# Kernel optimization log

Hardware: AMD Instinct MI355X
Metric: run time of the kernel (lower is better)

Reference implementation:

```python
import jax, jax.numpy as jnp
import numpy as np

INF = 10000000000000.0
HEADS = 12
HEAD_SIZE = 64

def _rope_tables(seqlen, dim):
    inv_freq = 1.0 / (10000.0 ** (jnp.arange(0, dim, 2, dtype=jnp.float32) / dim))
    t = jnp.arange(seqlen, dtype=jnp.float32)
    freqs = t[:, None] * inv_freq[None, :]            # [S, d/2]
    # unsqueeze_dim=-2 -> [S, 1, d/2] to broadcast over heads
    return jnp.sin(freqs)[:, None, :], jnp.cos(freqs)[:, None, :]

def _apply_rope(t, sin, cos):
    # t: [B, S, H, D]; sin/cos: [S, 1, D/2]
    t1, t2 = t[..., 0::2], t[..., 1::2]
    out = jnp.stack([t1 * cos - t2 * sin, t1 * sin + t2 * cos], axis=-1)
    return out.reshape(t.shape)

def setup_inputs() -> dict:
    key = jax.random.key(0)
    k1, k2 = jax.random.split(key)
    B, S, Hd = 32, 512, 1024
    x = jax.random.normal(k1, (B, S, Hd), dtype=jnp.float32)
    W = jax.random.normal(k2, (Hd, HEADS * 2 * HEAD_SIZE), dtype=jnp.float32) * (1.0 / np.sqrt(Hd))
    b = jnp.zeros((HEADS * 2 * HEAD_SIZE,), dtype=jnp.float32)
    attention_mask = jnp.ones((B, S), dtype=jnp.int32)
    return {"x": x, "W": W, "b": b, "attention_mask": attention_mask}

def reference(x, W, b, attention_mask):
    B, S, _ = x.shape
    proj = x @ W + b                                   # [B, S, H*2*D]
    proj = proj.reshape(B, S, HEADS, 2, HEAD_SIZE)
    qw, kw = proj[..., 0, :], proj[..., 1, :]          # [B, S, H, D]
    sin, cos = _rope_tables(S, HEAD_SIZE)
    qw = _apply_rope(qw, sin, cos)
    kw = _apply_rope(kw, sin, cos)
    logits = jnp.einsum('bmhd,bnhd->bhmn', qw, kw)     # [B, H, S, S]
    am = attention_mask.astype(logits.dtype)
    pad_mask = 1.0 - am[:, None, None, :] * am[:, None, :, None]
    logits = logits - pad_mask * INF
    idx = jnp.arange(S)
    tril = (idx[:, None] > idx[None, :]).astype(logits.dtype)  # strictly lower triangle
    logits = logits - tril * INF
    return logits / (HEAD_SIZE ** 0.5)
```

## Files before the change

kernel.cpp:

```cpp
#include <hip/hip_runtime.h>
#include <hip/hip_bf16.h>
#include <cstdint>

#define HEADS 12
#define HEAD_SIZE 64
#define SEQ 512
#define HD 1024
#define NPROJ 1536
#define INF_VAL 1e13f

typedef __attribute__((ext_vector_type(8))) __bf16 bf16x8;
typedef __attribute__((ext_vector_type(4))) float f32x4;

__device__ __forceinline__ unsigned short f2bf(float f) {
    unsigned u = __float_as_uint(f);
    u += 0x7fffu + ((u >> 16) & 1u);
    return (unsigned short)(u >> 16);
}

__device__ __forceinline__ void gl_lds16(const unsigned short* g, unsigned short* l) {
    __builtin_amdgcn_global_load_lds(
        (const __attribute__((address_space(1))) unsigned int*)g,
        (__attribute__((address_space(3))) unsigned int*)l, 16, 0, 0);
}

__global__ void __launch_bounds__(256) convert_x(const float* __restrict__ x,
                                                 unsigned short* __restrict__ xb) {
    const int i = blockIdx.x * 256 + threadIdx.x;
    const float4* src = (const float4*)x;
    float4 v0 = src[i * 2 + 0];
    float4 v1 = src[i * 2 + 1];
    uint4 p;
    p.x = f2bf(v0.x) | ((unsigned)f2bf(v0.y) << 16);
    p.y = f2bf(v0.z) | ((unsigned)f2bf(v0.w) << 16);
    p.z = f2bf(v1.x) | ((unsigned)f2bf(v1.y) << 16);
    p.w = f2bf(v1.z) | ((unsigned)f2bf(v1.w) << 16);
    ((uint4*)xb)[i] = p;
}

__global__ void __launch_bounds__(256) transpose_cast_w(const float* __restrict__ W,
                                                        unsigned short* __restrict__ Wt) {
    __shared__ unsigned short tile[64][65];
    const int bx = blockIdx.x;
    const int k0 = (bx & 15) * 64;
    const int n0 = (bx >> 4) * 64;
    const int t = threadIdx.x;
    const int tr = t >> 4;
    const int tc = (t & 15) * 4;
#pragma unroll
    for (int i = 0; i < 4; ++i) {
        int kk = tr + i * 16;
        float4 v = *(const float4*)&W[(size_t)(k0 + kk) * NPROJ + n0 + tc];
        tile[kk][tc + 0] = f2bf(v.x);
        tile[kk][tc + 1] = f2bf(v.y);
        tile[kk][tc + 2] = f2bf(v.z);
        tile[kk][tc + 3] = f2bf(v.w);
    }
    __syncthreads();
#pragma unroll
    for (int i = 0; i < 4; ++i) {
        int nn = tr + i * 16;
        ushort4 o;
        o.x = tile[tc + 0][nn];
        o.y = tile[tc + 1][nn];
        o.z = tile[tc + 2][nn];
        o.w = tile[tc + 3][nn];
        *(ushort4*)&Wt[(size_t)(n0 + nn) * HD + k0 + tc] = o;
    }
}

__global__ void __launch_bounds__(256) rope_table(float2* __restrict__ tab) {
    const int e = blockIdx.x * 256 + threadIdx.x;
    const int srow = e >> 5;
    const int fi = e & 31;
    float invf = __expf(-(float)fi * (0.03125f * 9.210340371976184f));
    float theta = (float)srow * invf;
    float sv, cv;
    __sincosf(theta, &sv, &cv);
    tab[e] = make_float2(sv, cv);
}

__global__ void __launch_bounds__(256) gemm1_rope(const unsigned short* __restrict__ xb,
                                                  const unsigned short* __restrict__ Wt,
                                                  const float* __restrict__ bias,
                                                  const float2* __restrict__ tab,
                                                  unsigned short* __restrict__ qws,
                                                  unsigned short* __restrict__ kws) {
    __shared__ __align__(16) char smem[32768];
    unsigned short* Alds = (unsigned short*)smem;
    unsigned short* Blds = (unsigned short*)(smem + 8192);

    const int bx = blockIdx.x;
    const int tile_m = bx / HEADS;
    const int h = bx - tile_m * HEADS;
    const int m0 = tile_m * 128;
    const int n0 = h * 128;

    const int t = threadIdx.x;
    const int w = t >> 6;
    const int lane = t & 63;
    const int wm = w >> 1;
    const int wn = w & 1;
    const int c16 = lane & 15;
    const int quad = lane >> 4;

    const int row0 = w * 32 + (lane >> 2);
    const int celem = (lane & 3) * 8;
    const unsigned short* ga0 = xb + (size_t)(m0 + row0) * HD + celem;
    const unsigned short* ga1 = xb + (size_t)(m0 + row0 + 16) * HD + celem;
    const unsigned short* gb0 = Wt + (size_t)(n0 + row0) * HD + celem;
    const unsigned short* gb1 = Wt + (size_t)(n0 + row0 + 16) * HD + celem;
    unsigned short* la0 = Alds + row0 * 32 + celem;
    unsigned short* la1 = Alds + (row0 + 16) * 32 + celem;
    unsigned short* lb0 = Blds + row0 * 32 + celem;
    unsigned short* lb1 = Blds + (row0 + 16) * 32 + celem;

    f32x4 acc[4][4];
#pragma unroll
    for (int i = 0; i < 4; ++i)
#pragma unroll
        for (int j = 0; j < 4; ++j) acc[i][j] = (f32x4){0.f, 0.f, 0.f, 0.f};

    for (int kt = 0; kt < HD; kt += 32) {
        gl_lds16(ga0 + kt, la0);
        gl_lds16(ga1 + kt, la1);
        gl_lds16(gb0 + kt, lb0);
        gl_lds16(gb1 + kt, lb1);
        __syncthreads();

        bf16x8 af[4], bfr[4];
#pragma unroll
        for (int mi = 0; mi < 4; ++mi)
            af[mi] = *(const bf16x8*)((char*)Alds + (wm * 64 + mi * 16 + c16) * 64 + quad * 16);
#pragma unroll
        for (int ni = 0; ni < 4; ++ni)
            bfr[ni] = *(const bf16x8*)((char*)Blds + (wn * 64 + ni * 16 + c16) * 64 + quad * 16);
#pragma unroll
        for (int mi = 0; mi < 4; ++mi)
#pragma unroll
            for (int ni = 0; ni < 4; ++ni)
                acc[mi][ni] = __builtin_amdgcn_mfma_f32_16x16x32_bf16(af[mi], bfr[ni], acc[mi][ni], 0, 0, 0);
        __syncthreads();
    }

    float bv[4];
#pragma unroll
    for (int ni = 0; ni < 4; ++ni) bv[ni] = bias[n0 + wn * 64 + ni * 16 + c16];

    const int bb = m0 >> 9;
    const int sbase = m0 & (SEQ - 1);
    const int odd = c16 & 1;
    const float sgn = odd ? 1.f : -1.f;
    unsigned short* outp = wn ? kws : qws;
    const size_t obase = ((size_t)(bb * HEADS + h) * SEQ + sbase) * HEAD_SIZE;

#pragma unroll
    for (int mi = 0; mi < 4; ++mi) {
#pragma unroll
        for (int ni = 0; ni < 4; ++ni) {
            const int d = ni * 16 + c16;
            const int fi = d >> 1;
#pragma unroll
            for (int r = 0; r < 4; ++r) {
                const int srow = wm * 64 + mi * 16 + quad * 4 + r;
                float v = acc[mi][ni][r] + bv[ni];
                float p = __shfl_xor(v, 1, 64);
                float2 sc = tab[(sbase + srow) * 32 + fi];
                float o = v * sc.y + sgn * p * sc.x;
                float o2 = __shfl_xor(o, 1, 64);
                if (!odd) {
                    unsigned pk;
                    asm("v_cvt_pk_bf16_f32 %0, %1, %2" : "=v"(pk) : "v"(o), "v"(o2));
                    *(unsigned*)&outp[obase + (size_t)srow * HEAD_SIZE + d] = pk;
                }
            }
        }
    }
}

__global__ void __launch_bounds__(256) gemm2_mask(const unsigned short* __restrict__ qws,
                                                  const unsigned short* __restrict__ kws,
                                                  const int* __restrict__ am,
                                                  float* __restrict__ out) {
    const int bh = blockIdx.y;
    const int b = bh / HEADS;
    const int tm = (blockIdx.x >> 2) * 128;
    const int tn = (blockIdx.x & 3) * 128;
    const int t = threadIdx.x;
    const int w = t >> 6, lane = t & 63;
    const int wm = w >> 1, wn = w & 1;
    const int c16 = lane & 15, quad = lane >> 4;

    const unsigned short* qp = qws + (size_t)bh * SEQ * HEAD_SIZE;
    const unsigned short* kp = kws + (size_t)bh * SEQ * HEAD_SIZE;

    f32x4 acc[4][4];
#pragma unroll
    for (int i = 0; i < 4; ++i)
#pragma unroll
        for (int j = 0; j < 4; ++j) acc[i][j] = (f32x4){0.f, 0.f, 0.f, 0.f};

#pragma unroll
    for (int ks = 0; ks < 2; ++ks) {
        bf16x8 af[4], bfr[4];
#pragma unroll
        for (int mi = 0; mi < 4; ++mi)
            af[mi] = *(const bf16x8*)(qp + (size_t)(tm + wm * 64 + mi * 16 + c16) * HEAD_SIZE
                                         + ks * 32 + quad * 8);
#pragma unroll
        for (int ni = 0; ni < 4; ++ni)
            bfr[ni] = *(const bf16x8*)(kp + (size_t)(tn + wn * 64 + ni * 16 + c16) * HEAD_SIZE
                                          + ks * 32 + quad * 8);
#pragma unroll
        for (int mi = 0; mi < 4; ++mi)
#pragma unroll
            for (int ni = 0; ni < 4; ++ni)
                acc[mi][ni] = __builtin_amdgcn_mfma_f32_16x16x32_bf16(bfr[ni], af[mi], acc[mi][ni], 0, 0, 0);
    }

    const int* amb = am + b * SEQ;
    float ammv[4];
#pragma unroll
    for (int mi = 0; mi < 4; ++mi) ammv[mi] = (float)amb[tm + wm * 64 + mi * 16 + c16];

#pragma unroll
    for (int ni = 0; ni < 4; ++ni) {
        const int nb = tn + wn * 64 + ni * 16 + quad * 4;
        const int4 a4 = *(const int4*)&amb[nb];
        const float an0 = (float)a4.x, an1 = (float)a4.y, an2 = (float)a4.z, an3 = (float)a4.w;
#pragma unroll
        for (int mi = 0; mi < 4; ++mi) {
            const int m = tm + wm * 64 + mi * 16 + c16;
            const float amm = ammv[mi];
            f32x4 o;
            o[0] = (acc[mi][ni][0] - ((1.0f - amm * an0) + ((m > nb + 0) ? 1.0f : 0.0f)) * INF_VAL) * 0.125f;
            o[1] = (acc[mi][ni][1] - ((1.0f - amm * an1) + ((m > nb + 1) ? 1.0f : 0.0f)) * INF_VAL) * 0.125f;
            o[2] = (acc[mi][ni][2] - ((1.0f - amm * an2) + ((m > nb + 2) ? 1.0f : 0.0f)) * INF_VAL) * 0.125f;
            o[3] = (acc[mi][ni][3] - ((1.0f - amm * an3) + ((m > nb + 3) ? 1.0f : 0.0f)) * INF_VAL) * 0.125f;
            __builtin_nontemporal_store(o, (f32x4*)&out[((size_t)bh * SEQ + m) * SEQ + nb]);
        }
    }
}

extern "C" void kernel_launch(void* const* d_in, const int* in_sizes, int n_in,
                              void* d_out, int out_size, void* d_ws, size_t ws_size,
                              hipStream_t stream) {
    (void)in_sizes; (void)n_in; (void)out_size; (void)ws_size;
    const float* x = (const float*)d_in[0];
    const float* W = (const float*)d_in[1];
    const float* bias = (const float*)d_in[2];
    const int* am = (const int*)d_in[3];
    float* out = (float*)d_out;

    unsigned short* Wt  = (unsigned short*)d_ws;
    unsigned short* qws = (unsigned short*)((char*)d_ws + 3145728);
    unsigned short* kws = (unsigned short*)((char*)d_ws + 3145728 + 25165824);
    unsigned short* xb  = (unsigned short*)((char*)d_ws + 3145728 + 2 * 25165824);
    float2* tab = (float2*)((char*)d_ws + 3145728 + 2 * 25165824 + 33554432);

    hipLaunchKernelGGL(convert_x, dim3(8192), dim3(256), 0, stream, x, xb);
    hipLaunchKernelGGL(transpose_cast_w, dim3(384), dim3(256), 0, stream, W, Wt);
    hipLaunchKernelGGL(rope_table, dim3(64), dim3(256), 0, stream, tab);
    hipLaunchKernelGGL(gemm1_rope, dim3(128 * HEADS), dim3(256), 0, stream, xb, Wt, bias, tab, qws, kws);
    hipLaunchKernelGGL(gemm2_mask, dim3(16, 32 * HEADS), dim3(256), 0, stream, qws, kws, am, out);
}
```

Baseline: 568.3 us.

## Double GEMM1 K-tile to 64 and swizzle block order across XCDs

The projection GEMM now loads 64-wide K slices per iteration instead of 32, which halves the number of barrier pairs and loop iterations and issues more MFMAs per sync. Both kernels remap block indices so that consecutive blocks scheduled round-robin onto the eight XCDs work on nearby tiles, aiming for better L2 reuse. The cost is twice the LDS per stage and row strides of 128 bytes in LDS, which may raise bank conflicts on the fragment reads. The swizzle also assumes the grid sizes are exactly 1536 and 12288 blocks.

Result: slower. 597.6 us (+5.2%).

```diff
diff --git a/kernel.cpp b/kernel.cpp
--- a/kernel.cpp
+++ b/kernel.cpp
@@ -88,9 +88,10 @@
                                                   unsigned short* __restrict__ kws) {
     __shared__ __align__(16) char smem[32768];
     unsigned short* Alds = (unsigned short*)smem;
-    unsigned short* Blds = (unsigned short*)(smem + 8192);
-
-    const int bx = blockIdx.x;
+    unsigned short* Blds = (unsigned short*)(smem + 16384);
+
+    const int bx0 = blockIdx.x;
+    const int bx = (bx0 & 7) * 192 + (bx0 >> 3);
     const int tile_m = bx / HEADS;
     const int h = bx - tile_m * HEADS;
     const int m0 = tile_m * 128;
@@ -104,16 +105,19 @@
     const int c16 = lane & 15;
     const int quad = lane >> 4;
 
-    const int row0 = w * 32 + (lane >> 2);
-    const int celem = (lane & 3) * 8;
-    const unsigned short* ga0 = xb + (size_t)(m0 + row0) * HD + celem;
-    const unsigned short* ga1 = xb + (size_t)(m0 + row0 + 16) * HD + celem;
-    const unsigned short* gb0 = Wt + (size_t)(n0 + row0) * HD + celem;
-    const unsigned short* gb1 = Wt + (size_t)(n0 + row0 + 16) * HD + celem;
-    unsigned short* la0 = Alds + row0 * 32 + celem;
-    unsigned short* la1 = Alds + (row0 + 16) * 32 + celem;
-    unsigned short* lb0 = Blds + row0 * 32 + celem;
-    unsigned short* lb1 = Blds + (row0 + 16) * 32 + celem;
+    const int srow0 = w * 32 + (lane >> 3);
+    const int scel = (lane & 7) * 8;
+    const unsigned short* gA[4];
+    const unsigned short* gB[4];
+    unsigned short* lA[4];
+    unsigned short* lB[4];
+#pragma unroll
+    for (int j = 0; j < 4; ++j) {
+        gA[j] = xb + (size_t)(m0 + srow0 + j * 8) * HD + scel;
+        gB[j] = Wt + (size_t)(n0 + srow0 + j * 8) * HD + scel;
+        lA[j] = Alds + (srow0 + j * 8) * 64 + scel;
+        lB[j] = Blds + (srow0 + j * 8) * 64 + scel;
+    }
 
     f32x4 acc[4][4];
 #pragma unroll
@@ -121,25 +125,29 @@
 #pragma unroll
         for (int j = 0; j < 4; ++j) acc[i][j] = (f32x4){0.f, 0.f, 0.f, 0.f};
 
-    for (int kt = 0; kt < HD; kt += 32) {
-        gl_lds16(ga0 + kt, la0);
-        gl_lds16(ga1 + kt, la1);
-        gl_lds16(gb0 + kt, lb0);
-        gl_lds16(gb1 + kt, lb1);
+    for (int kt = 0; kt < HD; kt += 64) {
+#pragma unroll
+        for (int j = 0; j < 4; ++j) {
+            gl_lds16(gA[j] + kt, lA[j]);
+            gl_lds16(gB[j] + kt, lB[j]);
+        }
         __syncthreads();
 
-        bf16x8 af[4], bfr[4];
-#pragma unroll
-        for (int mi = 0; mi < 4; ++mi)
-            af[mi] = *(const bf16x8*)((char*)Alds + (wm * 64 + mi * 16 + c16) * 64 + quad * 16);
-#pragma unroll
-        for (int ni = 0; ni < 4; ++ni)
-            bfr[ni] = *(const bf16x8*)((char*)Blds + (wn * 64 + ni * 16 + c16) * 64 + quad * 16);
-#pragma unroll
-        for (int mi = 0; mi < 4; ++mi)
+#pragma unroll
+        for (int ks = 0; ks < 2; ++ks) {
+            bf16x8 af[4], bfr[4];
+#pragma unroll
+            for (int mi = 0; mi < 4; ++mi)
+                af[mi] = *(const bf16x8*)((char*)Alds + (wm * 64 + mi * 16 + c16) * 128 + ks * 64 + quad * 16);
 #pragma unroll
             for (int ni = 0; ni < 4; ++ni)
-                acc[mi][ni] = __builtin_amdgcn_mfma_f32_16x16x32_bf16(af[mi], bfr[ni], acc[mi][ni], 0, 0, 0);
+                bfr[ni] = *(const bf16x8*)((char*)Blds + (wn * 64 + ni * 16 + c16) * 128 + ks * 64 + quad * 16);
+#pragma unroll
+            for (int mi = 0; mi < 4; ++mi)
+#pragma unroll
+                for (int ni = 0; ni < 4; ++ni)
+                    acc[mi][ni] = __builtin_amdgcn_mfma_f32_16x16x32_bf16(af[mi], bfr[ni], acc[mi][ni], 0, 0, 0);
+        }
         __syncthreads();
     }
 
@@ -182,10 +190,13 @@
                                                   const unsigned short* __restrict__ kws,
                                                   const int* __restrict__ am,
                                                   float* __restrict__ out) {
-    const int bh = blockIdx.y;
+    const int lin = blockIdx.y * 16 + blockIdx.x;
+    const int swz = (lin & 7) * 768 + (lin >> 3);
+    const int bh = swz >> 4;
+    const int tile = swz & 15;
     const int b = bh / HEADS;
-    const int tm = (blockIdx.x >> 2) * 128;
-    const int tn = (blockIdx.x & 3) * 128;
+    const int tm = (tile >> 2) * 128;
+    const int tn = (tile & 3) * 128;
     const int t = threadIdx.x;
     const int w = t >> 6, lane = t & 63;
     const int wm = w >> 1, wn = w & 1;
```
